# Kernel tuning notes

Hardware: AMD Instinct MI355X
Metric: run time of the kernel (lower is better)

Reference implementation:

```python
import jax, jax.numpy as jnp
import numpy as np

B, T, IN, H, L, P = 512, 512, 1, 100, 4, 0.5  # batch, seq, input, hidden, layers, dropout


def setup_inputs() -> dict:
    key = jax.random.key(0)
    ks = jax.random.split(key, 12)
    k = 1.0 / np.sqrt(H)  # torch nn.LSTM init scale
    u = lambda kk, shape: jax.random.uniform(kk, shape, jnp.float32, -k, k)
    inp = {
        "x": jax.random.normal(ks[0], (B, T, IN), jnp.float32),
        "W_ih0": u(ks[1], (4 * H, IN)),          # layer 0 input weights
        "W_ih_rest": u(ks[2], (L - 1, 4 * H, H)),  # layers 1..3 input weights
        "W_hh": u(ks[3], (L, 4 * H, H)),
        "b_ih": u(ks[4], (L, 4 * H)),
        "b_hh": u(ks[5], (L, 4 * H)),
        "W_out": u(ks[6], (1, H)),
        "b_out": u(ks[7], (1,)),
        # inter-layer dropout keep-masks (torch applies dropout to outputs of layers 0..L-2)
        "drop_masks": jax.random.bernoulli(ks[8], 1.0 - P, (L - 1, B, T, H)).astype(jnp.float32),
    }
    return inp


def _lstm_layer(seq, Wih, Whh, b):
    # seq: [T, B, in_dim]; returns [T, B, H]. PyTorch gate order: i, f, g, o.
    h0 = jnp.zeros((seq.shape[1], Whh.shape[-1]), seq.dtype)

    def step(carry, xt):
        h, c = carry
        gates = xt @ Wih.T + h @ Whh.T + b  # [B, 4H]
        i, f, g, o = jnp.split(gates, 4, axis=-1)
        c = jax.nn.sigmoid(f) * c + jax.nn.sigmoid(i) * jnp.tanh(g)
        h = jax.nn.sigmoid(o) * jnp.tanh(c)
        return (h, c), h

    _, hs = jax.lax.scan(step, (h0, h0), seq)
    return hs


def reference(x, W_ih0, W_ih_rest, W_hh, b_ih, b_hh, W_out, b_out, drop_masks):
    scale = 1.0 / (1.0 - P)
    seq = jnp.swapaxes(x, 0, 1)  # [T, B, IN] (batch_first -> time-major)
    seq = _lstm_layer(seq, W_ih0, W_hh[0], b_ih[0] + b_hh[0])
    for l in range(1, L):
        seq = seq * (jnp.swapaxes(drop_masks[l - 1], 0, 1) * scale)
        seq = _lstm_layer(seq, W_ih_rest[l - 1], W_hh[l], b_ih[l] + b_hh[l])
    last = seq[-1]  # [B, H] == lstm_out[:, -1]
    return last @ W_out.T + b_out  # [B, 1]
```

## Files before the change

kernel.cpp:

```cpp
#include <hip/hip_runtime.h>
#include <cstdint>
#include <cstddef>

#define BB 512
#define TT 512
#define HH 100
#define G4 400

template<bool IS_L0, bool WRITE_DROP>
__global__ __launch_bounds__(448, 1)
void rec_kernel(const float* __restrict__ x,
                const float* __restrict__ xc,
                const float* __restrict__ Whh_l,
                const float* __restrict__ Wih0,
                const float* __restrict__ bih_l,
                const float* __restrict__ bhh_l,
                const float* __restrict__ dmask_l,
                float* __restrict__ hdrop,
                float* __restrict__ st_h,
                float* __restrict__ st_c)
{
    __shared__ float hbuf[2][112][2];

    const int tid  = threadIdx.x;
    const int j    = tid >> 2;
    const int g    = tid & 3;
    const int pair = g >> 1;
    const int par  = g & 1;
    const bool active = (j < HH);
    const int jc   = active ? j : (HH - 1);
    const int rA   = pair * 100 + jc;
    const int rB   = rA + 200;
    const int b    = blockIdx.x * 2 + par;
    const bool isFO = (pair == 1);

    float wA[52], wB[52];
    {
        const int kb = par * 48;
        const float4* pa = (const float4*)(Whh_l + (size_t)rA * HH + kb);
        const float4* pb = (const float4*)(Whh_l + (size_t)rB * HH + kb);
        const int nf = 12 + par;
        #pragma unroll
        for (int m = 0; m < 13; ++m) {
            float4 va = {0.f, 0.f, 0.f, 0.f};
            float4 vb = {0.f, 0.f, 0.f, 0.f};
            if (m < nf) { va = pa[m]; vb = pb[m]; }
            wA[4 * m + 0] = va.x; wA[4 * m + 1] = va.y;
            wA[4 * m + 2] = va.z; wA[4 * m + 3] = va.w;
            wB[4 * m + 0] = vb.x; wB[4 * m + 1] = vb.y;
            wB[4 * m + 2] = vb.z; wB[4 * m + 3] = vb.w;
        }
    }

    float wxA = 0.f, wxB = 0.f, bsA = 0.f, bsB = 0.f;
    if (IS_L0) {
        wxA = Wih0[rA];  bsA = bih_l[rA] + bhh_l[rA];
        wxB = Wih0[rB];  bsB = bih_l[rB] + bhh_l[rB];
    }

    ((float*)hbuf)[tid] = 0.f;

    float c2 = 0.f, hlast = 0.f;
    __syncthreads();

    float ginA = 0.f, ginB = 0.f, xv = 0.f, mk = 0.f;
    if (IS_L0) {
        xv = x[(size_t)b * TT];
    } else {
        ginA = xc[(size_t)b * G4 + rA];
        ginB = xc[(size_t)b * G4 + rB];
    }
    if (WRITE_DROP && isFO && active) mk = dmask_l[(size_t)b * TT * HH + jc];

    int cur = 0;
    for (int t = 0; t < TT; ++t) {
        const int tn = (t + 1 < TT) ? (t + 1) : t;

        float nxv = 0.f, nginA = 0.f, nginB = 0.f, nmk = 0.f;
        if (IS_L0) {
            nxv = x[(size_t)b * TT + tn];
        } else {
            const size_t base = (size_t)tn * (BB * G4) + (size_t)b * G4;
            nginA = xc[base + rA];
            nginB = xc[base + rB];
        }
        if (WRITE_DROP && isFO && active)
            nmk = dmask_l[((size_t)b * TT + tn) * HH + jc];

        if (IS_L0) {
            ginA = fmaf(xv, wxA, bsA);
            ginB = fmaf(xv, wxB, bsB);
        }

        float aA0 = 0.f, aA1 = 0.f, aB0 = 0.f, aB1 = 0.f;
        {
            const float4* hp4 = (const float4*)&hbuf[cur][par * 48][0];
            #pragma unroll
            for (int m = 0; m < 26; ++m) {
                const float4 hv = hp4[m];
                aA0 = fmaf(wA[2 * m],     hv.x, aA0);
                aA1 = fmaf(wA[2 * m],     hv.y, aA1);
                aB0 = fmaf(wB[2 * m],     hv.x, aB0);
                aB1 = fmaf(wB[2 * m],     hv.y, aB1);
                aA0 = fmaf(wA[2 * m + 1], hv.z, aA0);
                aA1 = fmaf(wA[2 * m + 1], hv.w, aA1);
                aB0 = fmaf(wB[2 * m + 1], hv.z, aB0);
                aB1 = fmaf(wB[2 * m + 1], hv.w, aB1);
            }
        }

        const float sendA = par ? aA0 : aA1;
        const float keepA = par ? aA1 : aA0;
        const float totA  = keepA + __shfl_xor(sendA, 1) + ginA;
        const float sendB = par ? aB0 : aB1;
        const float keepB = par ? aB1 : aB0;
        const float totB  = keepB + __shfl_xor(sendB, 1) + ginB;

        const float eA   = __expf(-totA);
        const float sA   = 1.f / (1.f + eA);
        const float eB   = __expf(isFO ? (-totB) : (totB + totB));
        const float rB_  = 1.f / (1.f + eB);
        const float actB = isFO ? rB_ : fmaf(-2.f, rB_, 1.f);

        const float ship  = sA * actB;
        const float recvP = __shfl_xor(ship, 2);

        const int nxt = cur ^ 1;
        if (isFO) {
            c2 = fmaf(sA, c2, recvP);
            const float Ec = __expf(c2 + c2);
            const float th = 1.f - 2.f / (Ec + 1.f);
            const float h  = actB * th;
            hlast = h;
            if (active) {
                hbuf[nxt][j][par] = h;
                if (WRITE_DROP)
                    hdrop[((size_t)t * BB + b) * HH + j] = h * mk * 2.f;
            }
        }
        __syncthreads();
        cur = nxt;
        ginA = nginA; ginB = nginB; xv = nxv; mk = nmk;
    }

    if (isFO && active) {
        st_h[(size_t)b * HH + j] = hlast;
        st_c[(size_t)b * HH + j] = c2;
    }
}

__global__ __launch_bounds__(256, 2)
void xc_gemm(const float* __restrict__ A,
             const float* __restrict__ W,
             const float* __restrict__ bih_l,
             const float* __restrict__ bhh_l,
             float* __restrict__ xc)
{
    __shared__ float At[HH][132];
    __shared__ float Bt[HH][68];

    const int tid = threadIdx.x;
    const int n0  = blockIdx.x * 64;
    const size_t m0 = (size_t)blockIdx.y * 128;

    for (int s = tid; s < 128 * 25; s += 256) {
        const int r = s / 25, kq = s - r * 25;
        const float4 v = *(const float4*)&A[(m0 + r) * HH + kq * 4];
        At[kq * 4 + 0][r] = v.x; At[kq * 4 + 1][r] = v.y;
        At[kq * 4 + 2][r] = v.z; At[kq * 4 + 3][r] = v.w;
    }
    for (int s = tid; s < 64 * 25; s += 256) {
        const int r = s / 25, kq = s - r * 25;
        const int col = n0 + r;
        float4 v = {0.f, 0.f, 0.f, 0.f};
        if (col < G4) v = *(const float4*)&W[(size_t)col * HH + kq * 4];
        Bt[kq * 4 + 0][r] = v.x; Bt[kq * 4 + 1][r] = v.y;
        Bt[kq * 4 + 2][r] = v.z; Bt[kq * 4 + 3][r] = v.w;
    }
    __syncthreads();

    const int tx = tid & 15;
    const int ty = tid >> 4;
    float acc[8][4];
    #pragma unroll
    for (int i = 0; i < 8; ++i)
        #pragma unroll
        for (int jj = 0; jj < 4; ++jj) acc[i][jj] = 0.f;

    #pragma unroll 4
    for (int k = 0; k < HH; ++k) {
        const float4 a0 = *(const float4*)&At[k][ty * 8];
        const float4 a1 = *(const float4*)&At[k][ty * 8 + 4];
        const float4 bv = *(const float4*)&Bt[k][tx * 4];
        const float av[8] = {a0.x, a0.y, a0.z, a0.w, a1.x, a1.y, a1.z, a1.w};
        #pragma unroll
        for (int i = 0; i < 8; ++i) {
            acc[i][0] = fmaf(av[i], bv.x, acc[i][0]);
            acc[i][1] = fmaf(av[i], bv.y, acc[i][1]);
            acc[i][2] = fmaf(av[i], bv.z, acc[i][2]);
            acc[i][3] = fmaf(av[i], bv.w, acc[i][3]);
        }
    }

    const int col = n0 + tx * 4;
    if (col < G4) {
        const float4 u = *(const float4*)&bih_l[col];
        const float4 v = *(const float4*)&bhh_l[col];
        const float4 bias = {u.x + v.x, u.y + v.y, u.z + v.z, u.w + v.w};
        #pragma unroll
        for (int i = 0; i < 8; ++i) {
            const size_t r = m0 + ty * 8 + i;
            float4 o = {acc[i][0] + bias.x, acc[i][1] + bias.y,
                        acc[i][2] + bias.z, acc[i][3] + bias.w};
            *(float4*)&xc[r * G4 + col] = o;
        }
    }
}

__global__ __launch_bounds__(256)
void out_kernel(const float* __restrict__ st_h3,
                const float* __restrict__ Wout,
                const float* __restrict__ bout,
                float* __restrict__ out)
{
    const int b = blockIdx.x * 256 + threadIdx.x;
    if (b < BB) {
        float sum = bout[0];
        #pragma unroll 4
        for (int k = 0; k < HH; ++k)
            sum = fmaf(st_h3[(size_t)b * HH + k], Wout[k], sum);
        out[b] = sum;
    }
}

extern "C" void kernel_launch(void* const* d_in, const int* in_sizes, int n_in,
                              void* d_out, int out_size, void* d_ws, size_t ws_size,
                              hipStream_t stream)
{
    const float* x     = (const float*)d_in[0];
    const float* Wih0  = (const float*)d_in[1];
    const float* WihR  = (const float*)d_in[2];
    const float* Whh   = (const float*)d_in[3];
    const float* bih   = (const float*)d_in[4];
    const float* bhh   = (const float*)d_in[5];
    const float* Wout  = (const float*)d_in[6];
    const float* bout  = (const float*)d_in[7];
    const float* dmask = (const float*)d_in[8];
    float* out = (float*)d_out;

    float* ws    = (float*)d_ws;
    float* xcb   = ws;
    float* hdrop = xcb + (size_t)TT * BB * G4;
    float* sth   = hdrop + (size_t)TT * BB * HH;
    float* stc   = sth + (size_t)4 * BB * HH;

    const dim3 rgrid(BB / 2), rblk(448);
    const dim3 ggrid(7, (TT * BB) / 128), gblk(256);

    rec_kernel<true, true><<<rgrid, rblk, 0, stream>>>(
        x, nullptr, Whh, Wih0, bih, bhh, dmask,
        hdrop, sth, stc);
    for (int l = 1; l < 4; ++l) {
        xc_gemm<<<ggrid, gblk, 0, stream>>>(
            hdrop, WihR + (size_t)(l - 1) * G4 * HH,
            bih + l * G4, bhh + l * G4, xcb);
        if (l < 3) {
            rec_kernel<false, true><<<rgrid, rblk, 0, stream>>>(
                nullptr, xcb, Whh + (size_t)l * G4 * HH,
                nullptr, nullptr, nullptr,
                dmask + (size_t)l * BB * TT * HH,
                hdrop, sth + (size_t)l * BB * HH, stc + (size_t)l * BB * HH);
        } else {
            rec_kernel<false, false><<<rgrid, rblk, 0, stream>>>(
                nullptr, xcb, Whh + (size_t)l * G4 * HH,
                nullptr, nullptr, nullptr,
                nullptr,
                nullptr, sth + (size_t)l * BB * HH, stc + (size_t)l * BB * HH);
        }
    }
    out_kernel<<<dim3(2), dim3(256), 0, stream>>>(sth + (size_t)3 * BB * HH, Wout, bout, out);
}
```

Before: 3.751 ms.

## Batch LDS hidden-state loads before FMAs and use pointer-increment addressing

```diff
diff --git a/kernel.cpp b/kernel.cpp
--- a/kernel.cpp
+++ b/kernel.cpp
@@ -8,7 +8,7 @@
 #define G4 400
 
 template<bool IS_L0, bool WRITE_DROP>
-__global__ __launch_bounds__(448, 1)
+__global__ __attribute__((amdgpu_waves_per_eu(2, 2))) __launch_bounds__(448)
 void rec_kernel(const float* __restrict__ x,
                 const float* __restrict__ xc,
                 const float* __restrict__ Whh_l,
@@ -63,50 +63,63 @@
     float c2 = 0.f, hlast = 0.f;
     __syncthreads();
 
+    const float* pxcA = xc + (size_t)b * G4 + rA;
+    const float* pxcB = xc + (size_t)b * G4 + rB;
+    const float* pdm  = dmask_l ? (dmask_l + (size_t)b * TT * HH + jc) : nullptr;
+    const float* px   = x ? (x + (size_t)b * TT) : nullptr;
+
     float ginA = 0.f, ginB = 0.f, xv = 0.f, mk = 0.f;
     if (IS_L0) {
-        xv = x[(size_t)b * TT];
+        xv = px[0];
     } else {
-        ginA = xc[(size_t)b * G4 + rA];
-        ginB = xc[(size_t)b * G4 + rB];
-    }
-    if (WRITE_DROP && isFO && active) mk = dmask_l[(size_t)b * TT * HH + jc];
+        ginA = pxcA[0];
+        ginB = pxcB[0];
+    }
+    if (WRITE_DROP && isFO && active) mk = pdm[0];
 
     int cur = 0;
     for (int t = 0; t < TT; ++t) {
-        const int tn = (t + 1 < TT) ? (t + 1) : t;
+        const bool last = (t + 1 == TT);
+        const float* nxcA = last ? pxcA : pxcA + (size_t)BB * G4;
+        const float* nxcB = last ? pxcB : pxcB + (size_t)BB * G4;
+        const float* ndm  = (WRITE_DROP && isFO && active)
+                                ? (last ? pdm : pdm + HH) : pdm;
+        const float* npx  = IS_L0 ? (last ? px : px + 1) : px;
 
         float nxv = 0.f, nginA = 0.f, nginB = 0.f, nmk = 0.f;
         if (IS_L0) {
-            nxv = x[(size_t)b * TT + tn];
+            nxv = npx[0];
         } else {
-            const size_t base = (size_t)tn * (BB * G4) + (size_t)b * G4;
-            nginA = xc[base + rA];
-            nginB = xc[base + rB];
-        }
-        if (WRITE_DROP && isFO && active)
-            nmk = dmask_l[((size_t)b * TT + tn) * HH + jc];
+            nginA = nxcA[0];
+            nginB = nxcB[0];
+        }
+        if (WRITE_DROP && isFO && active) nmk = ndm[0];
 
         if (IS_L0) {
             ginA = fmaf(xv, wxA, bsA);
             ginB = fmaf(xv, wxB, bsB);
         }
 
-        float aA0 = 0.f, aA1 = 0.f, aB0 = 0.f, aB1 = 0.f;
+        float4 hv[26];
         {
             const float4* hp4 = (const float4*)&hbuf[cur][par * 48][0];
             #pragma unroll
-            for (int m = 0; m < 26; ++m) {
-                const float4 hv = hp4[m];
-                aA0 = fmaf(wA[2 * m],     hv.x, aA0);
-                aA1 = fmaf(wA[2 * m],     hv.y, aA1);
-                aB0 = fmaf(wB[2 * m],     hv.x, aB0);
-                aB1 = fmaf(wB[2 * m],     hv.y, aB1);
-                aA0 = fmaf(wA[2 * m + 1], hv.z, aA0);
-                aA1 = fmaf(wA[2 * m + 1], hv.w, aA1);
-                aB0 = fmaf(wB[2 * m + 1], hv.z, aB0);
-                aB1 = fmaf(wB[2 * m + 1], hv.w, aB1);
-            }
+            for (int m = 0; m < 26; ++m) hv[m] = hp4[m];
+        }
+        __builtin_amdgcn_sched_barrier(0);
+
+        float aA0 = 0.f, aA1 = 0.f, aB0 = 0.f, aB1 = 0.f;
+        #pragma unroll
+        for (int m = 0; m < 26; ++m) {
+            const float4 hvm = hv[m];
+            aA0 = fmaf(wA[2 * m],     hvm.x, aA0);
+            aA1 = fmaf(wA[2 * m],     hvm.y, aA1);
+            aB0 = fmaf(wB[2 * m],     hvm.x, aB0);
+            aB1 = fmaf(wB[2 * m],     hvm.y, aB1);
+            aA0 = fmaf(wA[2 * m + 1], hvm.z, aA0);
+            aA1 = fmaf(wA[2 * m + 1], hvm.w, aA1);
+            aB0 = fmaf(wB[2 * m + 1], hvm.z, aB0);
+            aB1 = fmaf(wB[2 * m + 1], hvm.w, aB1);
         }
 
         const float sendA = par ? aA0 : aA1;
@@ -141,6 +154,7 @@
         __syncthreads();
         cur = nxt;
         ginA = nginA; ginB = nginB; xv = nxv; mk = nmk;
+        pxcA = nxcA; pxcB = nxcB; pdm = ndm; px = npx;
     }
 
     if (isFO && active) {
```

After: 3.849 ms. 2.6% more time.
